# Kernel tuning notes

Measured on AMD Instinct MI355X. Metric: run time of the kernel, lower is better.

The kernel has to match this reference:

```python
import jax, jax.numpy as jnp
import numpy as np

B = 2000           # number of events (segments)
N = 1_000_000      # total points (sum of num_points)
D_IN, H, D_OUT = 16, 256, 128
EPS = 1e-5


def _layer_norm(x, g, b):
    m = x.mean(-1, keepdims=True)
    v = x.var(-1, keepdims=True)
    return (x - m) * jax.lax.rsqrt(v + EPS) * g + b


def setup_inputs() -> dict:
    key = jax.random.key(0)
    ks = jax.random.split(key, 8)
    # ragged counts, all positive, summing exactly to N
    rng = np.random.default_rng(0)
    counts = np.full(B, N // B, dtype=np.int64)
    d = rng.integers(-400, 401, size=B // 2)
    counts[: B // 2] += d
    counts[B // 2 :] -= d
    assert counts.sum() == N and (counts > 0).all()
    z_t = jax.random.normal(ks[0], (N, D_IN), dtype=jnp.float32)
    def lin(k, fi, fo):
        return jax.random.normal(k, (fi, fo), dtype=jnp.float32) / np.sqrt(fi)
    return {
        "z_t": z_t,
        "W1": lin(ks[1], D_IN, H), "b1": jnp.zeros((H,), jnp.float32),
        "g1": jnp.ones((H,), jnp.float32), "be1": jnp.zeros((H,), jnp.float32),
        "W2": lin(ks[2], H, H), "b2": jnp.zeros((H,), jnp.float32),
        "g2": jnp.ones((H,), jnp.float32), "be2": jnp.zeros((H,), jnp.float32),
        "W3": lin(ks[3], H, D_OUT), "b3": jnp.zeros((D_OUT,), jnp.float32),
        "num_points": jnp.asarray(counts, dtype=jnp.int64),
    }


def reference(z_t, W1, b1, g1, be1, W2, b2, g2, be2, W3, b3, num_points):
    # per-point phi MLP: Linear -> LN -> ReLU (x2) -> Linear
    h = jax.nn.relu(_layer_norm(z_t @ W1 + b1, g1, be1))
    h = jax.nn.relu(_layer_norm(h @ W2 + b2, g2, be2))
    phi = h @ W3 + b3                                  # [N, D_OUT]
    # fused ragged mean-pool + broadcast back (replaces split/stack/repeat_interleave)
    seg = jnp.repeat(jnp.arange(B), num_points, total_repeat_length=N)  # [N]
    sums = jax.ops.segment_sum(phi, seg, num_segments=B)                # [B, D_OUT]
    emb = sums / num_points[:, None].astype(phi.dtype)                  # mean pooling
    return emb[seg]                                                     # [N, D_OUT]
```

## Files before the change

kernel.cpp:

```cpp
#include <hip/hip_runtime.h>
#include <hip/hip_bf16.h>
#include <cstdint>
#include <cstddef>

#define NPTS  1000000
#define BSEG  2000
#define DIN   16
#define HDIM  256
#define DOUT  128
#define NTILE (NPTS / 32)
#define NWG   512

typedef __bf16          bf16x8 __attribute__((ext_vector_type(8)));
typedef unsigned short  us16x8 __attribute__((ext_vector_type(8)));
typedef unsigned int    u32x4  __attribute__((ext_vector_type(4)));
typedef float           f32x4  __attribute__((ext_vector_type(4)));
typedef float           f32x2  __attribute__((ext_vector_type(2)));

static __device__ __forceinline__ unsigned short f2bf(float x) {
    unsigned int u = __float_as_uint(x);
    u += 0x7fffu + ((u >> 16) & 1u);
    return (unsigned short)(u >> 16);
}

static __device__ __forceinline__ bf16x8 ldb8(const unsigned short* p) {
    u32x4 v = *(const u32x4*)p;
    return __builtin_bit_cast(bf16x8, v);
}
static __device__ __forceinline__ f32x4 mfma16(bf16x8 a, bf16x8 b, f32x4 c) {
    return __builtin_amdgcn_mfma_f32_16x16x32_bf16(a, b, c, 0, 0, 0);
}
static __device__ __forceinline__ void keep(bf16x8& v) {
    u32x4 u = __builtin_bit_cast(u32x4, v);
    unsigned a0 = u[0], a1 = u[1], a2 = u[2], a3 = u[3];
    asm volatile("" : "+v"(a0), "+v"(a1), "+v"(a2), "+v"(a3));
    u32x4 r; r[0] = a0; r[1] = a1; r[2] = a2; r[3] = a3;
    v = __builtin_bit_cast(bf16x8, r);
}

static __device__ __forceinline__ f32x2 pkadd(f32x2 a, f32x2 b) {
    f32x2 d; asm("v_pk_add_f32 %0, %1, %2" : "=v"(d) : "v"(a), "v"(b)); return d;
}
static __device__ __forceinline__ f32x2 pkmul(f32x2 a, f32x2 b) {
    f32x2 d; asm("v_pk_mul_f32 %0, %1, %2" : "=v"(d) : "v"(a), "v"(b)); return d;
}
static __device__ __forceinline__ f32x2 pkfma(f32x2 a, f32x2 b, f32x2 c) {
    f32x2 d; asm("v_pk_fma_f32 %0, %1, %2, %3" : "=v"(d) : "v"(a), "v"(b), "v"(c)); return d;
}
static __device__ __forceinline__ f32x2 relu2(f32x2 a) {
    f32x2 d; d[0] = fmaxf(a[0], 0.f); d[1] = fmaxf(a[1], 0.f); return d;
}
static __device__ __forceinline__ unsigned cvtpk(float a, float b) {
    unsigned d; asm("v_cvt_pk_bf16_f32 %0, %1, %2" : "=v"(d) : "v"(a), "v"(b)); return d;
}
static __device__ __forceinline__ f32x2 lohalf(f32x4 v) { return __builtin_shufflevector(v, v, 0, 1); }
static __device__ __forceinline__ f32x2 hihalf(f32x4 v) { return __builtin_shufflevector(v, v, 2, 3); }

static __device__ __forceinline__ float rsum16(float x) {
    x += __builtin_bit_cast(float, __builtin_amdgcn_update_dpp(
             0, __builtin_bit_cast(int, x), 0x128, 0xf, 0xf, false));
    x += __builtin_bit_cast(float, __builtin_amdgcn_update_dpp(
             0, __builtin_bit_cast(int, x), 0x124, 0xf, 0xf, false));
    x += __builtin_bit_cast(float, __builtin_amdgcn_update_dpp(
             0, __builtin_bit_cast(int, x), 0x122, 0xf, 0xf, false));
    x += __builtin_bit_cast(float, __builtin_amdgcn_update_dpp(
             0, __builtin_bit_cast(int, x), 0x121, 0xf, 0xf, false));
    return x;
}

__global__ __launch_bounds__(1024) void scan_counts(const int* __restrict__ counts,
                                                    int* __restrict__ offsets) {
    __shared__ int a[2048];
    const int t = threadIdx.x;
    a[t]        = (t        < BSEG) ? counts[t]        : 0;
    a[t + 1024] = (t + 1024 < BSEG) ? counts[t + 1024] : 0;
    for (int s = 1; s < 2048; s <<= 1) {
        __syncthreads();
        int x1 = (t >= s) ? a[t - s] : 0;
        int x2 = a[t + 1024 - s];
        __syncthreads();
        a[t] += x1;
        a[t + 1024] += x2;
    }
    __syncthreads();
    if (t == 0) offsets[0] = 0;
    offsets[t + 1] = a[t];
    if (t + 1024 < BSEG) offsets[t + 1025] = a[t + 1024];
}

__global__ __launch_bounds__(256) void fill_seg(const int* __restrict__ offsets,
                                                unsigned short* __restrict__ seg) {
    const int b  = blockIdx.x;
    const int lo = offsets[b], hi = offsets[b + 1];
    for (int i = lo + threadIdx.x; i < hi; i += 256) seg[i] = (unsigned short)b;
}

__global__ __launch_bounds__(256) void prep_weights(const float* __restrict__ W1,
                                                    const float* __restrict__ b1,
                                                    const float* __restrict__ W2,
                                                    unsigned short* __restrict__ w1t,
                                                    unsigned short* __restrict__ w2t) {
    const int i = blockIdx.x * 256 + threadIdx.x;
    if (i < HDIM * 32) {
        int n = i >> 5, k = i & 31;
        float v = (k < DIN) ? W1[k * HDIM + n] : ((k == DIN) ? b1[n] : 0.f);
        w1t[i] = f2bf(v);
    } else {
        int j = i - HDIM * 32;
        if (j < HDIM * HDIM) {
            int n = j >> 8, k = j & 255;
            w2t[j] = f2bf(W2[k * HDIM + n]);
        }
    }
}

__global__ __launch_bounds__(256, 2) void fused_phi_pool(
    const float* __restrict__ z,
    const unsigned short* __restrict__ w1t,
    const unsigned short* __restrict__ w2t,
    const float* __restrict__ g1, const float* __restrict__ be1,
    const float* __restrict__ b2, const float* __restrict__ g2, const float* __restrict__ be2,
    const unsigned short* __restrict__ seg,
    float* __restrict__ sums_h) {
    __shared__ __align__(16) unsigned short h1[32][264];
    __shared__ __align__(16) unsigned short w1l[HDIM * 32];
    __shared__ __align__(16) float part2[2][2][8][20];
    __shared__ int seg_sm[2][32];

    const int tid  = threadIdx.x;
    const int wave = tid >> 6;
    const int lane = tid & 63;
    const int l15  = lane & 15;
    const int quad = lane >> 4;
    const int colw = wave * 64 + l15;
    const bool zlane = (quad < 2);

    {
        const u32x4* src = (const u32x4*)w1t;
        u32x4* dst = (u32x4*)w1l;
        for (int i = tid; i < HDIM * 32 / 8; i += 256) dst[i] = src[i];
    }

    bf16x8 bw2[4][8];
#pragma unroll
    for (int t = 0; t < 4; ++t) {
        const int n = (wave * 4 + t) * 16 + l15;
#pragma unroll
        for (int ks = 0; ks < 8; ++ks) {
            bw2[t][ks] = ldb8(w2t + n * 256 + ks * 32 + quad * 8);
            keep(bw2[t][ks]);
        }
    }

    f32x2 gd1[4], ed1[4], gd2[4], ed2[4], bd2[4];
#pragma unroll
    for (int t = 0; t < 4; ++t) {
        const int c = colw + t * 16;
        float gv = g1[c];  gd1[t][0] = gv; gd1[t][1] = gv;
        float ev = be1[c]; ed1[t][0] = ev; ed1[t][1] = ev;
        float g2v = g2[c]; gd2[t][0] = g2v; gd2[t][1] = g2v;
        float e2v = be2[c]; ed2[t][0] = e2v; ed2[t][1] = e2v;
        float b2v = b2[c]; bd2[t][0] = b2v; bd2[t][1] = b2v;
    }
    const f32x2 zero2 = {0.f, 0.f};
    const unsigned h1w = (unsigned)(size_t)&h1[quad * 4][colw];

    float4 zn[2][2];
    {
        const int base0 = blockIdx.x * 32;
        if (zlane) {
#pragma unroll
            for (int mb = 0; mb < 2; ++mb) {
                const float* zp = z + (size_t)(base0 + mb * 16 + l15) * DIN + quad * 8;
                zn[mb][0] = *(const float4*)zp;
                zn[mb][1] = *(const float4*)(zp + 4);
            }
        }
    }

    __syncthreads();

    int p = 0;
    for (int tile = blockIdx.x; tile < NTILE; tile += NWG, p ^= 1) {
        const int base = tile * 32;
        if (tid < 32) seg_sm[p][tid] = (int)seg[base + tid];

        float4 zc[2][2];
#pragma unroll
        for (int mb = 0; mb < 2; ++mb) { zc[mb][0] = zn[mb][0]; zc[mb][1] = zn[mb][1]; }
        const int ntile = tile + NWG;
        if (zlane && ntile < NTILE) {
            const int nb = ntile * 32;
#pragma unroll
            for (int mb = 0; mb < 2; ++mb) {
                const float* zp = z + (size_t)(nb + mb * 16 + l15) * DIN + quad * 8;
                zn[mb][0] = *(const float4*)zp;
                zn[mb][1] = *(const float4*)(zp + 4);
            }
        }

        bf16x8 w1f[4];
#pragma unroll
        for (int t = 0; t < 4; ++t)
            w1f[t] = ldb8(&w1l[((wave * 4 + t) * 16 + l15) * 32 + quad * 8]);

        f32x4 a1[2][4];
#pragma unroll
        for (int mb = 0; mb < 2; ++mb) {
            bf16x8 af;
            if (zlane) {
                u32x4 u;
                u[0] = cvtpk(zc[mb][0].x, zc[mb][0].y);
                u[1] = cvtpk(zc[mb][0].z, zc[mb][0].w);
                u[2] = cvtpk(zc[mb][1].x, zc[mb][1].y);
                u[3] = cvtpk(zc[mb][1].z, zc[mb][1].w);
                af = __builtin_bit_cast(bf16x8, u);
            } else {
                u32x4 u = {(quad == 2) ? 0x3F80u : 0u, 0u, 0u, 0u};
                af = __builtin_bit_cast(bf16x8, u);
            }
            const f32x4 zero = {0.f, 0.f, 0.f, 0.f};
#pragma unroll
            for (int t = 0; t < 4; ++t) a1[mb][t] = mfma16(af, w1f[t], zero);
        }

#pragma unroll
        for (int mb = 0; mb < 2; ++mb)
#pragma unroll
            for (int rp = 0; rp < 2; ++rp) {
                f32x2 sv = zero2, qv = zero2;
#pragma unroll
                for (int t = 0; t < 4; ++t) {
                    f32x2 y = rp ? hihalf(a1[mb][t]) : lohalf(a1[mb][t]);
                    sv = pkadd(sv, y);
                    qv = pkfma(y, y, qv);
                }
                float sa = rsum16(sv[0]), sb = rsum16(sv[1]);
                float qa = rsum16(qv[0]), qb = rsum16(qv[1]);
                if (l15 == 0) {
                    f32x2 s2 = {sa, sb};
                    f32x2 q2 = {qa, qb};
                    *(f32x2*)&part2[p][mb][quad * 2 + rp][wave * 2]     = s2;
                    *(f32x2*)&part2[p][mb][quad * 2 + rp][8 + wave * 2] = q2;
                }
            }
        __syncthreads();

#pragma unroll
        for (int mb = 0; mb < 2; ++mb)
#pragma unroll
            for (int rp = 0; rp < 2; ++rp) {
                const float* pr = &part2[p][mb][quad * 2 + rp][0];
                f32x4 sa4 = *(const f32x4*)pr;
                f32x4 sb4 = *(const f32x4*)(pr + 4);
                f32x4 qa4 = *(const f32x4*)(pr + 8);
                f32x4 qb4 = *(const f32x4*)(pr + 12);
                f32x2 st2 = pkadd(pkadd(lohalf(sa4), hihalf(sa4)),
                                  pkadd(lohalf(sb4), hihalf(sb4)));
                f32x2 qt2 = pkadd(pkadd(lohalf(qa4), hihalf(qa4)),
                                  pkadd(lohalf(qb4), hihalf(qb4)));
                float m0 = st2[0] * (1.f / 256.f), m1 = st2[1] * (1.f / 256.f);
                float v0 = fmaf(qt2[0], 1.f / 256.f, -(m0 * m0));
                float v1 = fmaf(qt2[1], 1.f / 256.f, -(m1 * m1));
                float r0 = rsqrtf(fmaxf(v0, 0.f) + 1e-5f);
                float r1 = rsqrtf(fmaxf(v1, 0.f) + 1e-5f);
                f32x2 rs2 = {r0, r1};
                f32x2 mn2 = {-m0, -m1};
#pragma unroll
                for (int t = 0; t < 4; ++t) {
                    f32x2 A2 = pkmul(rs2, gd1[t]);
                    f32x2 C2 = pkfma(mn2, A2, ed1[t]);
                    f32x2 y  = rp ? hihalf(a1[mb][t]) : lohalf(a1[mb][t]);
                    f32x2 h2 = relu2(pkfma(y, A2, C2));
                    unsigned pkv  = cvtpk(h2[0], h2[1]);
                    unsigned addr = h1w + (unsigned)(mb * 8448 + rp * 1056 + t * 32);
                    asm volatile("ds_write_b16 %0, %1\n\t"
                                 "ds_write_b16_d16_hi %0, %1 offset:528"
                                 :: "v"(addr), "v"(pkv));
                }
            }
        __syncthreads();

        f32x4 a2[2][4];
#pragma unroll
        for (int mb = 0; mb < 2; ++mb) {
            const f32x4 zero = {0.f, 0.f, 0.f, 0.f};
#pragma unroll
            for (int t = 0; t < 4; ++t) a2[mb][t] = zero;
#pragma unroll
            for (int ks = 0; ks < 8; ++ks) {
                bf16x8 af = ldb8(&h1[mb * 16 + l15][ks * 32 + quad * 8]);
#pragma unroll
                for (int t = 0; t < 4; ++t) a2[mb][t] = mfma16(af, bw2[t][ks], a2[mb][t]);
            }
        }
#pragma unroll
        for (int mb = 0; mb < 2; ++mb)
#pragma unroll
            for (int rp = 0; rp < 2; ++rp) {
                f32x2 sv = zero2, qv = zero2;
#pragma unroll
                for (int t = 0; t < 4; ++t) {
                    f32x2 y = pkadd(rp ? hihalf(a2[mb][t]) : lohalf(a2[mb][t]), bd2[t]);
                    sv = pkadd(sv, y);
                    qv = pkfma(y, y, qv);
                }
                float sa = rsum16(sv[0]), sb = rsum16(sv[1]);
                float qa = rsum16(qv[0]), qb = rsum16(qv[1]);
                if (l15 == 0) {
                    f32x2 s2 = {sa, sb};
                    f32x2 q2 = {qa, qb};
                    *(f32x2*)&part2[p][mb][quad * 2 + rp][wave * 2]     = s2;
                    *(f32x2*)&part2[p][mb][quad * 2 + rp][8 + wave * 2] = q2;
                }
            }
        __syncthreads();

#pragma unroll
        for (int mb = 0; mb < 2; ++mb)
#pragma unroll
            for (int rp = 0; rp < 2; ++rp) {
                const float* pr = &part2[p][mb][quad * 2 + rp][0];
                f32x4 sa4 = *(const f32x4*)pr;
                f32x4 sb4 = *(const f32x4*)(pr + 4);
                f32x4 qa4 = *(const f32x4*)(pr + 8);
                f32x4 qb4 = *(const f32x4*)(pr + 12);
                f32x2 st2 = pkadd(pkadd(lohalf(sa4), hihalf(sa4)),
                                  pkadd(lohalf(sb4), hihalf(sb4)));
                f32x2 qt2 = pkadd(pkadd(lohalf(qa4), hihalf(qa4)),
                                  pkadd(lohalf(qb4), hihalf(qb4)));
                float m0 = st2[0] * (1.f / 256.f), m1 = st2[1] * (1.f / 256.f);
                float v0 = fmaf(qt2[0], 1.f / 256.f, -(m0 * m0));
                float v1 = fmaf(qt2[1], 1.f / 256.f, -(m1 * m1));
                float r0 = rsqrtf(fmaxf(v0, 0.f) + 1e-5f);
                float r1 = rsqrtf(fmaxf(v1, 0.f) + 1e-5f);
                f32x2 rs2 = {r0, r1};
                f32x2 mn2 = {-m0, -m1};
#pragma unroll
                for (int t = 0; t < 4; ++t) {
                    f32x2 A2 = pkmul(rs2, gd2[t]);
                    f32x2 C2 = pkfma(mn2, A2, ed2[t]);
                    f32x2 y  = pkadd(rp ? hihalf(a2[mb][t]) : lohalf(a2[mb][t]), bd2[t]);
                    f32x2 h2 = relu2(pkfma(y, A2, C2));
                    a2[mb][t][rp * 2]     = h2[0];
                    a2[mb][t][rp * 2 + 1] = h2[1];
                }
            }

        const int s0  = seg_sm[p][0];
        const int s31 = seg_sm[p][31];
        if (s0 == s31) {
#pragma unroll
            for (int t = 0; t < 4; ++t) {
                float cs = a2[0][t][0] + a2[0][t][1] + a2[0][t][2] + a2[0][t][3]
                         + a2[1][t][0] + a2[1][t][1] + a2[1][t][2] + a2[1][t][3];
                cs += __shfl_xor(cs, 16, 64);
                cs += __shfl_xor(cs, 32, 64);
                if (quad == 0)
                    atomicAdd(&sums_h[s0 * HDIM + colw + t * 16], cs);
            }
        } else {
            const int* sgp = &seg_sm[p][0];
            float m0v[4], m1v[4];
#pragma unroll
            for (int r = 0; r < 4; ++r) {
                m0v[r] = (sgp[quad * 4 + r]      == s0) ? 1.f : 0.f;
                m1v[r] = (sgp[16 + quad * 4 + r] == s0) ? 1.f : 0.f;
            }
#pragma unroll
            for (int t = 0; t < 4; ++t) {
                float cs = 0.f, ca = 0.f;
#pragma unroll
                for (int r = 0; r < 4; ++r) {
                    cs += a2[0][t][r] + a2[1][t][r];
                    ca = fmaf(a2[0][t][r], m0v[r], ca);
                    ca = fmaf(a2[1][t][r], m1v[r], ca);
                }
                cs += __shfl_xor(cs, 16, 64);
                cs += __shfl_xor(cs, 32, 64);
                ca += __shfl_xor(ca, 16, 64);
                ca += __shfl_xor(ca, 32, 64);
                if (quad == 0) {
                    atomicAdd(&sums_h[s0  * HDIM + colw + t * 16], ca);
                    atomicAdd(&sums_h[s31 * HDIM + colw + t * 16], cs - ca);
                }
            }
        }
    }
}

__global__ __launch_bounds__(256) void emb_gemm(const float* __restrict__ sums_h,
                                                const float* __restrict__ W3,
                                                const float* __restrict__ b3,
                                                const int* __restrict__ counts,
                                                float* __restrict__ emb) {
    const int b = blockIdx.x * 2 + (threadIdx.x >> 7);
    const int o = threadIdx.x & 127;
    const float* sh = sums_h + b * HDIM;
    float acc = 0.f;
#pragma unroll 8
    for (int k = 0; k < HDIM; ++k) acc = fmaf(sh[k], W3[k * DOUT + o], acc);
    emb[b * DOUT + o] = acc / (float)counts[b] + b3[o];
}

__global__ __launch_bounds__(256) void broadcast_out(const float* __restrict__ emb,
                                                     const unsigned short* __restrict__ seg,
                                                     float* __restrict__ out) {
    const int idx = blockIdx.x * 256 + threadIdx.x;
    const int n = idx >> 5, c = idx & 31;
    const int s = seg[n];
    f32x4 v = ((const f32x4*)emb)[s * 32 + c];
    __builtin_nontemporal_store(v, (f32x4*)out + idx);
}

extern "C" void kernel_launch(void* const* d_in, const int* in_sizes, int n_in,
                              void* d_out, int out_size, void* d_ws, size_t ws_size,
                              hipStream_t stream) {
    const float* z   = (const float*)d_in[0];
    const float* W1  = (const float*)d_in[1];
    const float* b1  = (const float*)d_in[2];
    const float* g1  = (const float*)d_in[3];
    const float* be1 = (const float*)d_in[4];
    const float* W2  = (const float*)d_in[5];
    const float* b2  = (const float*)d_in[6];
    const float* g2  = (const float*)d_in[7];
    const float* be2 = (const float*)d_in[8];
    const float* W3  = (const float*)d_in[9];
    const float* b3  = (const float*)d_in[10];
    const int* counts = (const int*)d_in[11];
    float* out = (float*)d_out;

    char* ws = (char*)d_ws;
    float*          sums_h  = (float*)(ws);
    float*          emb     = (float*)(ws + 2048000);
    int*            offsets = (int*)  (ws + 3072000);
    unsigned short* seg     = (unsigned short*)(ws + 3080016);
    unsigned short* w1t     = (unsigned short*)(ws + 5080016);
    unsigned short* w2t     = (unsigned short*)(ws + 5096400);

    hipMemsetAsync(sums_h, 0, (size_t)BSEG * HDIM * sizeof(float), stream);
    scan_counts<<<1, 1024, 0, stream>>>(counts, offsets);
    fill_seg<<<BSEG, 256, 0, stream>>>(offsets, seg);
    prep_weights<<<(HDIM * 32 + HDIM * HDIM) / 256, 256, 0, stream>>>(W1, b1, W2, w1t, w2t);
    fused_phi_pool<<<NWG, 256, 0, stream>>>(z, w1t, w2t,
                                            g1, be1, b2, g2, be2,
                                            seg, sums_h);
    emb_gemm<<<BSEG / 2, 256, 0, stream>>>(sums_h, W3, b3, counts, emb);
    broadcast_out<<<NPTS * DOUT / 4 / 256, 256, 0, stream>>>(emb, seg, out);
}
```

Baseline: 937.6 us.

## Assign contiguous tile ranges per block and accumulate segment sums in registers

```diff
diff --git a/kernel.cpp b/kernel.cpp
--- a/kernel.cpp
+++ b/kernel.cpp
@@ -125,7 +125,6 @@
     __shared__ __align__(16) unsigned short h1[32][264];
     __shared__ __align__(16) unsigned short w1l[HDIM * 32];
     __shared__ __align__(16) float part2[2][2][8][20];
-    __shared__ int seg_sm[2][32];
 
     const int tid  = threadIdx.x;
     const int wave = tid >> 6;
@@ -165,38 +164,79 @@
     const f32x2 zero2 = {0.f, 0.f};
     const unsigned h1w = (unsigned)(size_t)&h1[quad * 4][colw];
 
+    const int bid = blockIdx.x;
+    const int cpb = NTILE / NWG, rem = NTILE % NWG;
+    const int t0 = bid * cpb + (bid < rem ? bid : rem);
+    const int t1 = t0 + cpb + (bid < rem ? 1 : 0);
+
     float4 zn[2][2];
-    {
-        const int base0 = blockIdx.x * 32;
-        if (zlane) {
-#pragma unroll
-            for (int mb = 0; mb < 2; ++mb) {
-                const float* zp = z + (size_t)(base0 + mb * 16 + l15) * DIN + quad * 8;
-                zn[mb][0] = *(const float4*)zp;
-                zn[mb][1] = *(const float4*)(zp + 4);
-            }
-        }
-    }
+    if (zlane) {
+#pragma unroll
+        for (int mb = 0; mb < 2; ++mb) {
+            const float* zp = z + (size_t)(t0 * 32 + mb * 16 + l15) * DIN + quad * 8;
+            zn[mb][0] = *(const float4*)zp;
+            zn[mb][1] = *(const float4*)(zp + 4);
+        }
+    }
+    int s0n  = (int)seg[t0 * 32];
+    int s31n = (int)seg[t0 * 32 + 31];
+
+    f32x2 acc2[4];
+#pragma unroll
+    for (int t = 0; t < 4; ++t) acc2[t] = zero2;
+    int cur_seg = s0n;
+
+    auto flush = [&](int sg) {
+#pragma unroll
+        for (int t = 0; t < 4; ++t) {
+            float cs = acc2[t][0] + acc2[t][1];
+            cs += __shfl_xor(cs, 16, 64);
+            cs += __shfl_xor(cs, 32, 64);
+            if (quad == 0) atomicAdd(&sums_h[sg * HDIM + colw + t * 16], cs);
+        }
+    };
 
     __syncthreads();
 
     int p = 0;
-    for (int tile = blockIdx.x; tile < NTILE; tile += NWG, p ^= 1) {
-        const int base = tile * 32;
-        if (tid < 32) seg_sm[p][tid] = (int)seg[base + tid];
-
-        float4 zc[2][2];
-#pragma unroll
-        for (int mb = 0; mb < 2; ++mb) { zc[mb][0] = zn[mb][0]; zc[mb][1] = zn[mb][1]; }
-        const int ntile = tile + NWG;
-        if (zlane && ntile < NTILE) {
-            const int nb = ntile * 32;
-#pragma unroll
-            for (int mb = 0; mb < 2; ++mb) {
-                const float* zp = z + (size_t)(nb + mb * 16 + l15) * DIN + quad * 8;
-                zn[mb][0] = *(const float4*)zp;
-                zn[mb][1] = *(const float4*)(zp + 4);
-            }
+    for (int tile = t0; tile < t1; ++tile, p ^= 1) {
+        const int s0c = s0n, s31c = s31n;
+
+        bf16x8 af[2];
+#pragma unroll
+        for (int mb = 0; mb < 2; ++mb) {
+            if (zlane) {
+                u32x4 u;
+                u[0] = cvtpk(zn[mb][0].x, zn[mb][0].y);
+                u[1] = cvtpk(zn[mb][0].z, zn[mb][0].w);
+                u[2] = cvtpk(zn[mb][1].x, zn[mb][1].y);
+                u[3] = cvtpk(zn[mb][1].z, zn[mb][1].w);
+                af[mb] = __builtin_bit_cast(bf16x8, u);
+            } else {
+                u32x4 u = {(quad == 2) ? 0x3F80u : 0u, 0u, 0u, 0u};
+                af[mb] = __builtin_bit_cast(bf16x8, u);
+            }
+        }
+
+        if (s0c != cur_seg) {
+            flush(cur_seg);
+#pragma unroll
+            for (int t = 0; t < 4; ++t) acc2[t] = zero2;
+            cur_seg = s0c;
+        }
+
+        if (tile + 1 < t1) {
+            const int nb = (tile + 1) * 32;
+            if (zlane) {
+#pragma unroll
+                for (int mb = 0; mb < 2; ++mb) {
+                    const float* zp = z + (size_t)(nb + mb * 16 + l15) * DIN + quad * 8;
+                    zn[mb][0] = *(const float4*)zp;
+                    zn[mb][1] = *(const float4*)(zp + 4);
+                }
+            }
+            s0n  = (int)seg[nb];
+            s31n = (int)seg[nb + 31];
         }
 
         bf16x8 w1f[4];
@@ -207,21 +247,9 @@
         f32x4 a1[2][4];
 #pragma unroll
         for (int mb = 0; mb < 2; ++mb) {
-            bf16x8 af;
-            if (zlane) {
-                u32x4 u;
-                u[0] = cvtpk(zc[mb][0].x, zc[mb][0].y);
-                u[1] = cvtpk(zc[mb][0].z, zc[mb][0].w);
-                u[2] = cvtpk(zc[mb][1].x, zc[mb][1].y);
-                u[3] = cvtpk(zc[mb][1].z, zc[mb][1].w);
-                af = __builtin_bit_cast(bf16x8, u);
-            } else {
-                u32x4 u = {(quad == 2) ? 0x3F80u : 0u, 0u, 0u, 0u};
-                af = __builtin_bit_cast(bf16x8, u);
-            }
             const f32x4 zero = {0.f, 0.f, 0.f, 0.f};
 #pragma unroll
-            for (int t = 0; t < 4; ++t) a1[mb][t] = mfma16(af, w1f[t], zero);
+            for (int t = 0; t < 4; ++t) a1[mb][t] = mfma16(af[mb], w1f[t], zero);
         }
 
 #pragma unroll
@@ -289,9 +317,9 @@
             for (int t = 0; t < 4; ++t) a2[mb][t] = zero;
 #pragma unroll
             for (int ks = 0; ks < 8; ++ks) {
-                bf16x8 af = ldb8(&h1[mb * 16 + l15][ks * 32 + quad * 8]);
-#pragma unroll
-                for (int t = 0; t < 4; ++t) a2[mb][t] = mfma16(af, bw2[t][ks], a2[mb][t]);
+                bf16x8 a = ldb8(&h1[mb * 16 + l15][ks * 32 + quad * 8]);
+#pragma unroll
+                for (int t = 0; t < 4; ++t) a2[mb][t] = mfma16(a, bw2[t][ks], a2[mb][t]);
             }
         }
 #pragma unroll
@@ -347,25 +375,22 @@
                 }
             }
 
-        const int s0  = seg_sm[p][0];
-        const int s31 = seg_sm[p][31];
-        if (s0 == s31) {
-#pragma unroll
-            for (int t = 0; t < 4; ++t) {
-                float cs = a2[0][t][0] + a2[0][t][1] + a2[0][t][2] + a2[0][t][3]
-                         + a2[1][t][0] + a2[1][t][1] + a2[1][t][2] + a2[1][t][3];
-                cs += __shfl_xor(cs, 16, 64);
-                cs += __shfl_xor(cs, 32, 64);
-                if (quad == 0)
-                    atomicAdd(&sums_h[s0 * HDIM + colw + t * 16], cs);
-            }
+        if (s0c == s31c) {
+#pragma unroll
+            for (int mb = 0; mb < 2; ++mb)
+#pragma unroll
+                for (int t = 0; t < 4; ++t)
+                    acc2[t] = pkadd(pkadd(acc2[t], lohalf(a2[mb][t])), hihalf(a2[mb][t]));
         } else {
-            const int* sgp = &seg_sm[p][0];
+            flush(cur_seg);
+#pragma unroll
+            for (int t = 0; t < 4; ++t) acc2[t] = zero2;
+            const int base = tile * 32;
             float m0v[4], m1v[4];
 #pragma unroll
             for (int r = 0; r < 4; ++r) {
-                m0v[r] = (sgp[quad * 4 + r]      == s0) ? 1.f : 0.f;
-                m1v[r] = (sgp[16 + quad * 4 + r] == s0) ? 1.f : 0.f;
+                m0v[r] = ((int)seg[base + quad * 4 + r]      == s0c) ? 1.f : 0.f;
+                m1v[r] = ((int)seg[base + 16 + quad * 4 + r] == s0c) ? 1.f : 0.f;
             }
 #pragma unroll
             for (int t = 0; t < 4; ++t) {
@@ -381,12 +406,14 @@
                 ca += __shfl_xor(ca, 16, 64);
                 ca += __shfl_xor(ca, 32, 64);
                 if (quad == 0) {
-                    atomicAdd(&sums_h[s0  * HDIM + colw + t * 16], ca);
-                    atomicAdd(&sums_h[s31 * HDIM + colw + t * 16], cs - ca);
-                }
-            }
-        }
-    }
+                    atomicAdd(&sums_h[s0c  * HDIM + colw + t * 16], ca);
+                    atomicAdd(&sums_h[s31c * HDIM + colw + t * 16], cs - ca);
+                }
+            }
+            cur_seg = s31c;
+        }
+    }
+    flush(cur_seg);
 }
 
 __global__ __launch_bounds__(256) void emb_gemm(const float* __restrict__ sums_h,
```

Result: slower. 974.4 us (+3.9%).
